# Performance work log

Measured on AMD Instinct MI355X. Metric: run time of the kernel, lower is better.

The kernel has to match this reference:

```python
import math
import jax, jax.numpy as jnp
import numpy as np

# ---- constants (module-level in the original source) ----
_CMAG_A = 0.75
_CMAG_B = 120.0
_CMAG_K = 17.3
_DEG2RAD = math.pi / 180.0
AMP = 100.0
_SPREAD = math.sqrt(AMP / 675.0)
VIEW_ANGLE = 90.0
MAP_SIZE = 256
SOFT_MATCH_SIGMA = 1.5
RENDER_CHUNK = 50
N_SHANK = 10            # N_CONTACTPOINTS_SHANK -> 10^3 = 1000 contacts
SPACING = 0.4           # SPACING_ALONG_XY (mm)


def setup_inputs() -> dict:
    key = jax.random.key(0)
    ks = jax.random.split(key, 12)
    B, V, N = 8, 10000, N_SHANK ** 3
    # bounded params: alpha, beta, offset, shank_length
    alpha = jax.random.uniform(ks[0], (B,), minval=-60.0, maxval=60.0)
    beta = jax.random.uniform(ks[1], (B,), minval=0.0, maxval=90.0)
    offset = jax.random.uniform(ks[2], (B,), minval=0.0, maxval=3.0)
    shank = jax.random.uniform(ks[3], (B,), minval=8.0, maxval=12.0)
    params = jnp.stack([alpha, beta, offset, shank], axis=-1).astype(jnp.float32)
    electrode_logits = jax.random.normal(ks[4], (B, N), dtype=jnp.float32)
    start_loc = jnp.array([30.0, -40.0, 10.0], dtype=jnp.float32)
    # V1 voxel positions clustered around the insertion start point
    v1_pos = start_loc + jax.random.uniform(ks[5], (V, 3), minval=-25.0, maxval=25.0)
    pol = jax.random.uniform(ks[6], (V,), minval=0.0, maxval=360.0)
    ecc = jax.random.uniform(ks[7], (V,), minval=0.2, maxval=12.0)
    sig = jax.random.uniform(ks[8], (V,), minval=0.5, maxval=3.0)
    v1_prf = jnp.stack([pol, ecc, sig], axis=-1).astype(jnp.float32)
    surf_dist_lut = jax.random.uniform(ks[9], (37, 26), minval=10.0, maxval=20.0)
    alpha_grid = jnp.linspace(-90.0, 90.0, 37, dtype=jnp.float32)
    beta_grid = jnp.linspace(-15.0, 110.0, 26, dtype=jnp.float32)
    # contact grid template [n^3, 3] = (x, y, z_frac)
    yv = jnp.arange(N_SHANK, dtype=jnp.float32) * SPACING
    xv = jnp.arange(N_SHANK, dtype=jnp.float32) * SPACING
    zf = jnp.linspace(0.0, 1.0, N_SHANK, dtype=jnp.float32)
    yy, xx, zz = jnp.meshgrid(yv, xv, zf, indexing='ij')
    grid_template = jnp.stack([xx, yy, zz], axis=-1).reshape(-1, 3)
    return {
        'params': params,
        'electrode_logits': electrode_logits,
        'v1_pos': v1_pos.astype(jnp.float32),
        'v1_prf': v1_prf,
        'start_loc': start_loc,
        'surf_dist_lut': surf_dist_lut.astype(jnp.float32),
        'alpha_grid': alpha_grid,
        'beta_grid': beta_grid,
        'grid_template': grid_template,
    }


def _rotation_matrix(alpha_deg, beta_deg):
    a = alpha_deg * _DEG2RAD
    b = beta_deg * _DEG2RAD
    ca, sa = jnp.cos(a), jnp.sin(a)
    cb, sb = jnp.cos(b), jnp.sin(b)
    ones = jnp.ones_like(a)
    zeros = jnp.zeros_like(a)
    Rx = jnp.stack([jnp.stack([ones, zeros, zeros], -1),
                    jnp.stack([zeros, ca, -sa], -1),
                    jnp.stack([zeros, sa, ca], -1)], axis=-2)
    Ry = jnp.stack([jnp.stack([cb, zeros, sb], -1),
                    jnp.stack([zeros, ones, zeros], -1),
                    jnp.stack([-sb, zeros, cb], -1)], axis=-2)
    return Rx @ Ry  # [B,3,3]


def _interp_surface_dist(alpha, beta, lut, a_grid, b_grid):
    # bilinear grid_sample with align_corners=True + border padding == clamped
    # pixel-space bilinear interpolation
    na, nb = lut.shape
    a_norm = 2.0 * (alpha - a_grid[0]) / (a_grid[-1] - a_grid[0] + 1e-08) - 1.0
    b_norm = 2.0 * (beta - b_grid[0]) / (b_grid[-1] - b_grid[0] + 1e-08) - 1.0
    ai = jnp.clip((a_norm + 1.0) * 0.5 * (na - 1), 0.0, na - 1.0)
    bi = jnp.clip((b_norm + 1.0) * 0.5 * (nb - 1), 0.0, nb - 1.0)
    a0 = jnp.clip(jnp.floor(ai), 0, na - 1).astype(jnp.int32)
    b0 = jnp.clip(jnp.floor(bi), 0, nb - 1).astype(jnp.int32)
    a1 = jnp.minimum(a0 + 1, na - 1)
    b1 = jnp.minimum(b0 + 1, nb - 1)
    fa = ai - a0.astype(ai.dtype)
    fb = bi - b0.astype(bi.dtype)
    v00 = lut[a0, b0]; v01 = lut[a0, b1]; v10 = lut[a1, b0]; v11 = lut[a1, b1]
    out = (v00 * (1 - fa) * (1 - fb) + v01 * (1 - fa) * fb
           + v10 * fa * (1 - fb) + v11 * fa * fb)
    return jnp.maximum(out, 1.0)


def _forward(params, electrode_logits, v1_pos, v1_prf, start_loc,
             surf_dist_lut, alpha_grid, beta_grid, grid_template):
    B = params.shape[0]
    N = grid_template.shape[0]
    H = W = MAP_SIZE
    alpha, beta, offset, shank = (params[:, 0], params[:, 1], params[:, 2], params[:, 3])
    elec_prob = jax.nn.sigmoid(electrode_logits)

    # ---- positioned contact grid [B,N,3] ----
    xy = jnp.broadcast_to(grid_template[None, :, :2], (B, N, 2))
    z = grid_template[None, :, 2:3] * shank[:, None, None]
    grid = jnp.concatenate([xy, z], axis=-1)
    grid = grid - grid.mean(axis=1, keepdims=True)
    R = _rotation_matrix(alpha, beta)
    rotated = jnp.einsum('bnc,bdc->bnd', grid, R)   # grid @ R^T
    ref = jnp.array([0.0, 0.0, -1.0], dtype=params.dtype)
    direction = jnp.einsum('bij,j->bi', R, ref)
    direction = direction / jnp.linalg.norm(direction, axis=-1, keepdims=True)
    surf_dist = _interp_surface_dist(alpha, beta, surf_dist_lut, alpha_grid, beta_grid)
    penetration = surf_dist - shank / 2.0 - offset
    grid_center = start_loc[None, :] + direction * penetration[:, None]
    contact_pos = rotated + grid_center[:, None, :]

    # ---- soft PRF lookup via gaussian kernel matching (avoid [B,N,V,3] diff) ----
    p2 = jnp.sum(contact_pos ** 2, axis=-1)          # [B,N]
    v2 = jnp.sum(v1_pos ** 2, axis=-1)               # [V]
    cross = jnp.einsum('bnc,vc->bnv', contact_pos, v1_pos)
    d2 = jnp.maximum(p2[:, :, None] + v2[None, None, :] - 2.0 * cross, 0.0)
    weights = jnp.exp(-d2 / (2.0 * SOFT_MATCH_SIGMA ** 2))   # [B,N,V]
    wsum = weights.sum(axis=-1)
    validity = jnp.minimum(wsum, 1.0)
    weights_norm = weights / (wsum[:, :, None] + 1e-08)
    prf = jnp.einsum('bnv,vp->bnp', weights_norm, v1_prf)    # [B,N,3]

    # ---- chunked gaussian splatting -> [B,1,H,W] ----
    angle_rad = prf[:, :, 0] * _DEG2RAD
    ecc = prf[:, :, 1]
    m = _CMAG_K * (1.0 / (ecc + _CMAG_A) - 1.0 / (ecc + _CMAG_B))
    m_inv = 1.0 / (jnp.abs(m) + 1e-08)
    phos_sigma = _SPREAD * m_inv / 2.0
    scaled_ecc = H / VIEW_ANGLE
    cx = ecc * jnp.cos(angle_rad) * scaled_ecc + H / 2.0
    cy = ecc * jnp.sin(angle_rad) * scaled_ecc + W / 2.0
    phos_size = jnp.maximum(phos_sigma * scaled_ecc, 1.0)
    w = elec_prob * validity

    gy, gx = jnp.meshgrid(jnp.arange(H, dtype=params.dtype),
                          jnp.arange(W, dtype=params.dtype), indexing='ij')
    n_chunks = N // RENDER_CHUNK
    def to_chunks(t):  # [B,N] -> [n_chunks,B,chunk]
        return t.reshape(B, n_chunks, RENDER_CHUNK).transpose(1, 0, 2)
    scan_in = (to_chunks(cx), to_chunks(cy), to_chunks(phos_size), to_chunks(w))

    def body(acc, ch):
        cx_, cy_, s_, w_ = ch  # [B,chunk]
        g = jnp.exp(-((gx[None, None] - cx_[:, :, None, None]) ** 2
                      + (gy[None, None] - cy_[:, :, None, None]) ** 2)
                    / (s_[:, :, None, None] ** 2 + 1e-08))
        return acc + jnp.einsum('bchw,bc->bhw', g, w_), None

    phos_map, _ = jax.lax.scan(body, jnp.zeros((B, H, W), dtype=params.dtype), scan_in)
    phos_map = jnp.rot90(phos_map, k=1, axes=(-2, -1))
    max_val = phos_map.reshape(B, -1).max(axis=1)[:, None, None]
    phos_map = phos_map / (max_val + 1e-08)
    return phos_map[:, None, :, :]


def reference(params, electrode_logits, v1_pos, v1_prf, start_loc,
              surf_dist_lut, alpha_grid, beta_grid, grid_template):
    return _forward(params, electrode_logits, v1_pos, v1_prf, start_loc,
                    surf_dist_lut, alpha_grid, beta_grid, grid_template)
```

## Files before the change

### kernel.cpp

```cpp
#include <hip/hip_runtime.h>
#include <math.h>

#define WS_MAP    0
#define WS_CNT    524416
#define WS_EPOS   524736
#define WS_CPOS   557504
#define WS_CPRF   885184
#define WS_PART   1049024
#define WS_MAX    1704384

#define NB 8
#define NN 1000
#define NV 10000
#define NSEG 40
#define NSEG2 20
#define SEGCAP 256
#define NEB 1024

__global__ __launch_bounds__(256) void k_cull(const float* __restrict__ params,
                                              const float* __restrict__ start_loc,
                                              const float* __restrict__ lut,
                                              const float* __restrict__ agrid,
                                              const float* __restrict__ bgrid,
                                              const float* __restrict__ v1_pos,
                                              const float* __restrict__ v1_prf,
                                              const float* __restrict__ tmpl,
                                              float* __restrict__ ws) {
    __shared__ float sst[NB*16];
    __shared__ int   lcnt[NB];
    int g = blockIdx.x, t = threadIdx.x;
    int v = g*256 + t;
    float4* mp = (float4*)(ws + WS_MAP);
    #pragma unroll
    for (int k = 0; k < 13; ++k) {
        int idx = k*10240 + v;
        if (idx < 131072) mp[idx] = make_float4(0.f,0.f,0.f,0.f);
    }
    if (g == 0 && t < NB) ws[WS_MAX + t] = 0.f;
    if (t < NB) lcnt[t] = 0;
    if (t < NB) {
        int b = t;
        float alpha = params[b*4+0], beta = params[b*4+1];
        float off   = params[b*4+2], shank = params[b*4+3];
        const float D2R = 0.017453292519943295f;
        float a = alpha*D2R, bb = beta*D2R;
        float ca = cosf(a), sa = sinf(a), cb = cosf(bb), sb = sinf(bb);
        float r00=cb,     r01=0.f, r02=sb;
        float r10=sa*sb,  r11=ca,  r12=-sa*cb;
        float r20=-ca*sb, r21=sa,  r22=ca*cb;
        float dx=-r02, dy=-r12, dz=-r22;
        float inv = rsqrtf(dx*dx+dy*dy+dz*dz);
        dx*=inv; dy*=inv; dz*=inv;
        float ag0=agrid[0], agN=agrid[36], bg0=bgrid[0], bgN=bgrid[25];
        float an = 2.f*(alpha-ag0)/(agN-ag0+1e-8f) - 1.f;
        float bn = 2.f*(beta -bg0)/(bgN-bg0+1e-8f) - 1.f;
        float ai = fminf(fmaxf((an+1.f)*0.5f*36.f, 0.f), 36.f);
        float bi = fminf(fmaxf((bn+1.f)*0.5f*25.f, 0.f), 25.f);
        int a0 = (int)floorf(ai); a0 = a0<0?0:(a0>36?36:a0);
        int b0 = (int)floorf(bi); b0 = b0<0?0:(b0>25?25:b0);
        int a1 = a0+1>36?36:a0+1;
        int b1 = b0+1>25?25:b0+1;
        float fa = ai - (float)a0, fb = bi - (float)b0;
        float v00=lut[a0*26+b0], v01=lut[a0*26+b1], v10=lut[a1*26+b0], v11=lut[a1*26+b1];
        float sd = v00*(1.f-fa)*(1.f-fb) + v01*(1.f-fa)*fb + v10*fa*(1.f-fb) + v11*fa*fb;
        sd = fmaxf(sd, 1.f);
        float pen = sd - shank*0.5f - off;
        float hs = shank*0.5f;
        sst[b*16+0]=r00; sst[b*16+1]=r01; sst[b*16+2]=r02;
        sst[b*16+3]=r10; sst[b*16+4]=r11; sst[b*16+5]=r12;
        sst[b*16+6]=r20; sst[b*16+7]=r21; sst[b*16+8]=r22;
        sst[b*16+9]  = start_loc[0] + dx*pen;
        sst[b*16+10] = start_loc[1] + dy*pen;
        sst[b*16+11] = start_loc[2] + dz*pen;
        sst[b*16+12] = shank;
        sst[b*16+13] = fabsf(r00)*1.8f + fabsf(r01)*1.8f + fabsf(r02)*hs;
        sst[b*16+14] = fabsf(r10)*1.8f + fabsf(r11)*1.8f + fabsf(r12)*hs;
        sst[b*16+15] = fabsf(r20)*1.8f + fabsf(r21)*1.8f + fabsf(r22)*hs;
    }
    __syncthreads();
    const float C = -0.32059889797532524f;
    if (v < 8192) {
        float4* ep = (float4*)(ws + WS_EPOS);
        if (v < NB*NN) {
            int b = v/1000, n = v - b*1000;
            const float* st = sst + b*16;
            float gx = tmpl[n*3]-1.8f, gy = tmpl[n*3+1]-1.8f;
            float gz = (tmpl[n*3+2]-0.5f)*st[12];
            float px = st[0]*gx + st[1]*gy + st[2]*gz + st[9];
            float py = st[3]*gx + st[4]*gy + st[5]*gz + st[10];
            float pz = st[6]*gx + st[7]*gy + st[8]*gz + st[11];
            ep[v] = make_float4(px, py, pz, C*(px*px+py*py+pz*pz));
        } else {
            ep[v] = make_float4(0.f, 0.f, 0.f, -1e30f);
        }
    }
    bool valid = v < NV;
    float x=0.f, y=0.f, z=0.f, pol=0.f, ecc=0.f;
    if (valid) {
        x = v1_pos[v*3]; y = v1_pos[v*3+1]; z = v1_pos[v*3+2];
        pol = v1_prf[v*3]; ecc = v1_prf[v*3+1];
    }
    float4 payload = make_float4(-2.f*C*x, -2.f*C*y, -2.f*C*z, C*(x*x+y*y+z*z));
    int lane = t & 63;
    float4* cpos = (float4*)(ws + WS_CPOS);
    float2* cprf = (float2*)(ws + WS_CPRF);
    #pragma unroll
    for (int b = 0; b < NB; ++b) {
        const float* st = sst + b*16;
        float dxc = fmaxf(fabsf(x - st[9])  - st[13], 0.f);
        float dyc = fmaxf(fabsf(y - st[10]) - st[14], 0.f);
        float dzc = fmaxf(fabsf(z - st[11]) - st[15], 0.f);
        bool pred = valid && (dxc*dxc + dyc*dyc + dzc*dzc <= 90.f);
        unsigned long long m = __ballot(pred);
        int base = 0;
        if (lane == 0) base = atomicAdd(&lcnt[b], (int)__popcll(m));
        base = __shfl(base, 0, 64);
        if (pred) {
            int my = base + (int)__popcll(m & ((1ull << lane) - 1ull));
            int slot = b*10240 + g*SEGCAP + my;
            cpos[slot] = payload;
            cprf[slot] = make_float2(pol, ecc);
        }
    }
    __syncthreads();
    if (t < NB) ((int*)(ws + WS_CNT))[g*NB + t] = lcnt[t];
}

__global__ __launch_bounds__(256) void k_match(float* __restrict__ ws) {
    __shared__ float4 sq[2*SEGCAP];
    __shared__ float2 spe[2*SEGCAP];
    int g = blockIdx.x, t = threadIdx.x;
    int b = g / 40, r = g - b*40, qp = r >> 1, eg = r & 1;
    int q0 = qp*2, q1 = qp*2 + 1;
    const int* cnt = (const int*)(ws + WS_CNT);
    int c0 = cnt[q0*NB + b], c1 = cnt[q1*NB + b];
    const float4* cpos = (const float4*)(ws + WS_CPOS);
    const float2* cprf = (const float2*)(ws + WS_CPRF);
    if (t < c0) {
        sq[t]  = cpos[b*10240 + q0*SEGCAP + t];
        spe[t] = cprf[b*10240 + q0*SEGCAP + t];
    }
    if (t < c1) {
        sq[c0 + t]  = cpos[b*10240 + q1*SEGCAP + t];
        spe[c0 + t] = cprf[b*10240 + q1*SEGCAP + t];
    }
    __syncthreads();
    int cq = c0 + c1;
    const float4* ep = (const float4*)(ws + WS_EPOS);
    int n0 = eg*512 + t, n1 = n0 + 256;
    float4 P0 = (n0 < NN) ? ep[b*NN + n0] : make_float4(0.f,0.f,0.f,-1e30f);
    float4 P1 = (n1 < NN) ? ep[b*NN + n1] : make_float4(0.f,0.f,0.f,-1e30f);
    float sw0=0.f,sp0=0.f,se0=0.f, sw1=0.f,sp1=0.f,se1=0.f;
    #pragma unroll 2
    for (int i = 0; i < cq; ++i) {
        float4 qq = sq[i];
        float2 pe = spe[i];
        float a0 = fmaf(qq.x, P0.x, fmaf(qq.y, P0.y, fmaf(qq.z, P0.z, P0.w + qq.w)));
        float w0 = __builtin_amdgcn_exp2f(a0);
        sw0 += w0; sp0 = fmaf(w0, pe.x, sp0); se0 = fmaf(w0, pe.y, se0);
        float a1 = fmaf(qq.x, P1.x, fmaf(qq.y, P1.y, fmaf(qq.z, P1.z, P1.w + qq.w)));
        float w1 = __builtin_amdgcn_exp2f(a1);
        sw1 += w1; sp1 = fmaf(w1, pe.x, sp1); se1 = fmaf(w1, pe.y, se1);
    }
    float4* part = (float4*)(ws + WS_PART);
    int baseq = (b*NSEG2 + qp)*NEB;
    part[baseq + n0] = make_float4(sw0, sp0, se0, 0.f);
    part[baseq + n1] = make_float4(sw1, sp1, se1, 0.f);
}

__global__ __launch_bounds__(256) void k_prender(const float* __restrict__ logits,
                                                 float* __restrict__ ws) {
    __shared__ float4 red[4][64];
    __shared__ float4 par[64];
    __shared__ float  mred[4];
    int g = blockIdx.x, t = threadIdx.x, lane = t & 63, w = t >> 6;
    int b = g >> 4, E0 = (g & 15) * 64;
    const float4* part = (const float4*)(ws + WS_PART);
    int el = E0 + lane;
    float sw = 0.f, sp = 0.f, se = 0.f;
    #pragma unroll
    for (int i = 0; i < 5; ++i) {
        float4 p = part[(b*NSEG2 + (w + i*4))*NEB + el];
        sw += p.x; sp += p.y; se += p.z;
    }
    red[w][lane] = make_float4(sw, sp, se, 0.f);
    __syncthreads();
    if (w == 0) {
        float4 a = red[0][lane], b4 = red[1][lane], c4 = red[2][lane], d4 = red[3][lane];
        sw = (a.x+b4.x) + (c4.x+d4.x);
        sp = (a.y+b4.y) + (c4.y+d4.y);
        se = (a.z+b4.z) + (c4.z+d4.z);
        float denom = sw + 1e-8f;
        float pol = sp/denom, eccv = se/denom;
        float validity = fminf(sw, 1.f);
        int n = E0 + lane;
        float lg = (n < NN) ? logits[b*NN + n] : 0.f;
        float prob = 1.f/(1.f + __expf(-lg));
        float wgt = (n < NN) ? prob * validity : 0.f;
        float ang = pol * 0.017453292519943295f;
        float m1 = 17.3f*(1.f/(eccv+0.75f) - 1.f/(eccv+120.f));
        float minv = 1.f/(fabsf(m1)+1e-8f);
        float sig  = 0.3849001794597506f * minv * 0.5f;
        const float scl = 256.f/90.f;
        float s = fmaxf(sig*scl, 1.f);
        float invden = 1.f/(s*s + 1e-8f);
        par[lane] = make_float4(eccv*__cosf(ang)*scl + 128.f,
                                eccv*__sinf(ang)*scl + 128.f, invden, wgt);
    }
    __syncthreads();
    int ix = lane & 7, iy = lane >> 3;
    float mx = 0.f;
    for (int k = 0; k < 16; ++k) {
        int el2 = k*4 + w;
        float4 P = par[el2];
        if (P.w <= 0.f) continue;
        int fx = (int)floorf(P.x), fy = (int)floorf(P.y);
        int X = fx - 3 + ix, Y = fy - 3 + iy;
        if (X >= 0 && X < 256 && Y >= 0 && Y < 256) {
            float dx = (float)X - P.x, dy = (float)Y - P.y;
            float d2 = dx*dx + dy*dy;
            if (d2 <= 12.25f) {
                float val = P.w * __expf(-d2 * P.z);
                float old = atomicAdd(ws + WS_MAP + b*65536 + Y*256 + X, val);
                mx = fmaxf(mx, old + val);
            }
        }
    }
    #pragma unroll
    for (int s2 = 32; s2 >= 1; s2 >>= 1) mx = fmaxf(mx, __shfl_xor(mx, s2, 64));
    if (lane == 0) mred[w] = mx;
    __syncthreads();
    if (t == 0) {
        mx = fmaxf(fmaxf(mred[0], mred[1]), fmaxf(mred[2], mred[3]));
        atomicMax((unsigned int*)(ws + WS_MAX + b), __float_as_uint(mx));
    }
}

__global__ __launch_bounds__(256) void k_final(const float* __restrict__ ws,
                                               float* __restrict__ out) {
    __shared__ float tile[32][33];
    int g  = blockIdx.x;
    int b  = g >> 6;
    int t6 = g & 63;
    int r0 = (t6 >> 3) * 32;
    int c0 = (t6 & 7) * 32;
    int ic0 = 224 - r0;
    int j  = threadIdx.x & 31;
    int i0 = threadIdx.x >> 5;
    const float* m = ws + WS_MAP + b*65536;
    #pragma unroll
    for (int p = 0; p < 4; ++p) {
        int i = i0 + p*8;
        tile[i][j] = m[(c0+i)*256 + ic0 + j];
    }
    __syncthreads();
    float inv = 1.f/(ws[WS_MAX + b] + 1e-8f);
    #pragma unroll
    for (int p = 0; p < 4; ++p) {
        int k = i0 + p*8;
        out[b*65536 + (r0+k)*256 + c0 + j] = tile[j][31-k] * inv;
    }
}

extern "C" void kernel_launch(void* const* d_in, const int* in_sizes, int n_in,
                              void* d_out, int out_size, void* d_ws, size_t ws_size,
                              hipStream_t stream) {
    const float* params    = (const float*)d_in[0];
    const float* logits    = (const float*)d_in[1];
    const float* v1_pos    = (const float*)d_in[2];
    const float* v1_prf    = (const float*)d_in[3];
    const float* start_loc = (const float*)d_in[4];
    const float* lut       = (const float*)d_in[5];
    const float* agrid     = (const float*)d_in[6];
    const float* bgrid     = (const float*)d_in[7];
    const float* tmpl      = (const float*)d_in[8];
    float* ws  = (float*)d_ws;
    float* out = (float*)d_out;

    k_cull   <<<40,  256, 0, stream>>>(params, start_loc, lut, agrid, bgrid,
                                       v1_pos, v1_prf, tmpl, ws);
    k_match  <<<320, 256, 0, stream>>>(ws);
    k_prender<<<128, 256, 0, stream>>>(logits, ws);
    k_final  <<<512, 256, 0, stream>>>(ws, out);
}
```

Measured before the change: 101.8 us.

## Fuse pipeline into one cooperative kernel with tile-local shared-memory splatting

Merges the four kernels (cull, match, prender, final) into a single cooperative launch of 320 blocks, with grid.sync between stages. The render stage now splats each block's 32x64 output tile into shared memory, using a per-tile culled element list, rather than doing global atomics into a zeroed map. This removes the full-map zeroing and the separate rotate/normalise pass. It aims to cut launch overhead and global atomic and memory traffic, at the cost of grid-wide barriers and fewer active blocks in the later stages.

```diff
diff --git a/kernel.cpp b/kernel.cpp
--- a/kernel.cpp
+++ b/kernel.cpp
@@ -1,13 +1,8 @@
 #include <hip/hip_runtime.h>
+#include <hip/hip_cooperative_groups.h>
 #include <math.h>
 
-#define WS_MAP    0
-#define WS_CNT    524416
-#define WS_EPOS   524736
-#define WS_CPOS   557504
-#define WS_CPRF   885184
-#define WS_PART   1049024
-#define WS_MAX    1704384
+namespace cg = cooperative_groups;
 
 #define NB 8
 #define NN 1000
@@ -17,248 +12,274 @@
 #define SEGCAP 256
 #define NEB 1024
 
-__global__ __launch_bounds__(256) void k_cull(const float* __restrict__ params,
-                                              const float* __restrict__ start_loc,
-                                              const float* __restrict__ lut,
-                                              const float* __restrict__ agrid,
-                                              const float* __restrict__ bgrid,
-                                              const float* __restrict__ v1_pos,
-                                              const float* __restrict__ v1_prf,
-                                              const float* __restrict__ tmpl,
-                                              float* __restrict__ ws) {
-    __shared__ float sst[NB*16];
-    __shared__ int   lcnt[NB];
-    int g = blockIdx.x, t = threadIdx.x;
-    int v = g*256 + t;
-    float4* mp = (float4*)(ws + WS_MAP);
-    #pragma unroll
-    for (int k = 0; k < 13; ++k) {
-        int idx = k*10240 + v;
-        if (idx < 131072) mp[idx] = make_float4(0.f,0.f,0.f,0.f);
-    }
-    if (g == 0 && t < NB) ws[WS_MAX + t] = 0.f;
-    if (t < NB) lcnt[t] = 0;
-    if (t < NB) {
-        int b = t;
-        float alpha = params[b*4+0], beta = params[b*4+1];
-        float off   = params[b*4+2], shank = params[b*4+3];
-        const float D2R = 0.017453292519943295f;
-        float a = alpha*D2R, bb = beta*D2R;
-        float ca = cosf(a), sa = sinf(a), cb = cosf(bb), sb = sinf(bb);
-        float r00=cb,     r01=0.f, r02=sb;
-        float r10=sa*sb,  r11=ca,  r12=-sa*cb;
-        float r20=-ca*sb, r21=sa,  r22=ca*cb;
-        float dx=-r02, dy=-r12, dz=-r22;
-        float inv = rsqrtf(dx*dx+dy*dy+dz*dz);
-        dx*=inv; dy*=inv; dz*=inv;
-        float ag0=agrid[0], agN=agrid[36], bg0=bgrid[0], bgN=bgrid[25];
-        float an = 2.f*(alpha-ag0)/(agN-ag0+1e-8f) - 1.f;
-        float bn = 2.f*(beta -bg0)/(bgN-bg0+1e-8f) - 1.f;
-        float ai = fminf(fmaxf((an+1.f)*0.5f*36.f, 0.f), 36.f);
-        float bi = fminf(fmaxf((bn+1.f)*0.5f*25.f, 0.f), 25.f);
-        int a0 = (int)floorf(ai); a0 = a0<0?0:(a0>36?36:a0);
-        int b0 = (int)floorf(bi); b0 = b0<0?0:(b0>25?25:b0);
-        int a1 = a0+1>36?36:a0+1;
-        int b1 = b0+1>25?25:b0+1;
-        float fa = ai - (float)a0, fb = bi - (float)b0;
-        float v00=lut[a0*26+b0], v01=lut[a0*26+b1], v10=lut[a1*26+b0], v11=lut[a1*26+b1];
-        float sd = v00*(1.f-fa)*(1.f-fb) + v01*(1.f-fa)*fb + v10*fa*(1.f-fb) + v11*fa*fb;
-        sd = fmaxf(sd, 1.f);
-        float pen = sd - shank*0.5f - off;
-        float hs = shank*0.5f;
-        sst[b*16+0]=r00; sst[b*16+1]=r01; sst[b*16+2]=r02;
-        sst[b*16+3]=r10; sst[b*16+4]=r11; sst[b*16+5]=r12;
-        sst[b*16+6]=r20; sst[b*16+7]=r21; sst[b*16+8]=r22;
-        sst[b*16+9]  = start_loc[0] + dx*pen;
-        sst[b*16+10] = start_loc[1] + dy*pen;
-        sst[b*16+11] = start_loc[2] + dz*pen;
-        sst[b*16+12] = shank;
-        sst[b*16+13] = fabsf(r00)*1.8f + fabsf(r01)*1.8f + fabsf(r02)*hs;
-        sst[b*16+14] = fabsf(r10)*1.8f + fabsf(r11)*1.8f + fabsf(r12)*hs;
-        sst[b*16+15] = fabsf(r20)*1.8f + fabsf(r21)*1.8f + fabsf(r22)*hs;
-    }
-    __syncthreads();
-    const float C = -0.32059889797532524f;
-    if (v < 8192) {
-        float4* ep = (float4*)(ws + WS_EPOS);
-        if (v < NB*NN) {
-            int b = v/1000, n = v - b*1000;
+#define WS_CNT  0
+#define WS_EPOS 512
+#define WS_CPOS 33280
+#define WS_CPRF 360960
+#define WS_PART 524800
+#define WS_PAR  1180160
+#define WS_MAX  1212928
+
+__global__ __launch_bounds__(256, 2) void k_fused(
+    const float* __restrict__ params,
+    const float* __restrict__ logits,
+    const float* __restrict__ v1_pos,
+    const float* __restrict__ v1_prf,
+    const float* __restrict__ start_loc,
+    const float* __restrict__ lut,
+    const float* __restrict__ agrid,
+    const float* __restrict__ bgrid,
+    const float* __restrict__ tmpl,
+    float* __restrict__ ws,
+    float* __restrict__ out)
+{
+    cg::grid_group grid = cg::this_grid();
+    __shared__ __align__(16) unsigned char smem[12544];
+    const int g = blockIdx.x, t = threadIdx.x;
+    const int lane = t & 63, w = t >> 6;
+
+    if (g < NSEG) {
+        float* sst = (float*)smem;
+        int*   lcnt = (int*)(smem + 512);
+        if (t < NB) lcnt[t] = 0;
+        if (t < NB) {
+            int b = t;
+            float alpha = params[b*4+0], beta = params[b*4+1];
+            float off   = params[b*4+2], shank = params[b*4+3];
+            const float D2R = 0.017453292519943295f;
+            float a = alpha*D2R, bb = beta*D2R;
+            float ca = cosf(a), sa = sinf(a), cb = cosf(bb), sb = sinf(bb);
+            float r00=cb,     r01=0.f, r02=sb;
+            float r10=sa*sb,  r11=ca,  r12=-sa*cb;
+            float r20=-ca*sb, r21=sa,  r22=ca*cb;
+            float dx=-r02, dy=-r12, dz=-r22;
+            float inv = rsqrtf(dx*dx+dy*dy+dz*dz);
+            dx*=inv; dy*=inv; dz*=inv;
+            float ag0=agrid[0], agN=agrid[36], bg0=bgrid[0], bgN=bgrid[25];
+            float an = 2.f*(alpha-ag0)/(agN-ag0+1e-8f) - 1.f;
+            float bn = 2.f*(beta -bg0)/(bgN-bg0+1e-8f) - 1.f;
+            float ai = fminf(fmaxf((an+1.f)*0.5f*36.f, 0.f), 36.f);
+            float bi = fminf(fmaxf((bn+1.f)*0.5f*25.f, 0.f), 25.f);
+            int a0 = (int)floorf(ai); a0 = a0<0?0:(a0>36?36:a0);
+            int b0 = (int)floorf(bi); b0 = b0<0?0:(b0>25?25:b0);
+            int a1 = a0+1>36?36:a0+1;
+            int b1 = b0+1>25?25:b0+1;
+            float fa = ai - (float)a0, fb = bi - (float)b0;
+            float v00=lut[a0*26+b0], v01=lut[a0*26+b1], v10=lut[a1*26+b0], v11=lut[a1*26+b1];
+            float sd = v00*(1.f-fa)*(1.f-fb) + v01*(1.f-fa)*fb + v10*fa*(1.f-fb) + v11*fa*fb;
+            sd = fmaxf(sd, 1.f);
+            float pen = sd - shank*0.5f - off;
+            float hs = shank*0.5f;
+            sst[b*16+0]=r00; sst[b*16+1]=r01; sst[b*16+2]=r02;
+            sst[b*16+3]=r10; sst[b*16+4]=r11; sst[b*16+5]=r12;
+            sst[b*16+6]=r20; sst[b*16+7]=r21; sst[b*16+8]=r22;
+            sst[b*16+9]  = start_loc[0] + dx*pen;
+            sst[b*16+10] = start_loc[1] + dy*pen;
+            sst[b*16+11] = start_loc[2] + dz*pen;
+            sst[b*16+12] = shank;
+            sst[b*16+13] = fabsf(r00)*1.8f + fabsf(r01)*1.8f + fabsf(r02)*hs;
+            sst[b*16+14] = fabsf(r10)*1.8f + fabsf(r11)*1.8f + fabsf(r12)*hs;
+            sst[b*16+15] = fabsf(r20)*1.8f + fabsf(r21)*1.8f + fabsf(r22)*hs;
+        }
+        __syncthreads();
+        const float C = -0.32059889797532524f;
+        int v = g*256 + t;
+        if (v < 8192) {
+            float4* ep = (float4*)(ws + WS_EPOS);
+            if (v < NB*NN) {
+                int b = v/1000, n = v - b*1000;
+                const float* st = sst + b*16;
+                float gx = tmpl[n*3]-1.8f, gy = tmpl[n*3+1]-1.8f;
+                float gz = (tmpl[n*3+2]-0.5f)*st[12];
+                float px = st[0]*gx + st[1]*gy + st[2]*gz + st[9];
+                float py = st[3]*gx + st[4]*gy + st[5]*gz + st[10];
+                float pz = st[6]*gx + st[7]*gy + st[8]*gz + st[11];
+                ep[v] = make_float4(px, py, pz, C*(px*px+py*py+pz*pz));
+            } else {
+                ep[v] = make_float4(0.f, 0.f, 0.f, -1e30f);
+            }
+        }
+        bool valid = v < NV;
+        float x=0.f, y=0.f, z=0.f, pol=0.f, ecc=0.f;
+        if (valid) {
+            x = v1_pos[v*3]; y = v1_pos[v*3+1]; z = v1_pos[v*3+2];
+            pol = v1_prf[v*3]; ecc = v1_prf[v*3+1];
+        }
+        float4 payload = make_float4(-2.f*C*x, -2.f*C*y, -2.f*C*z, C*(x*x+y*y+z*z));
+        float4* cpos = (float4*)(ws + WS_CPOS);
+        float2* cprf = (float2*)(ws + WS_CPRF);
+        #pragma unroll
+        for (int b = 0; b < NB; ++b) {
             const float* st = sst + b*16;
-            float gx = tmpl[n*3]-1.8f, gy = tmpl[n*3+1]-1.8f;
-            float gz = (tmpl[n*3+2]-0.5f)*st[12];
-            float px = st[0]*gx + st[1]*gy + st[2]*gz + st[9];
-            float py = st[3]*gx + st[4]*gy + st[5]*gz + st[10];
-            float pz = st[6]*gx + st[7]*gy + st[8]*gz + st[11];
-            ep[v] = make_float4(px, py, pz, C*(px*px+py*py+pz*pz));
-        } else {
-            ep[v] = make_float4(0.f, 0.f, 0.f, -1e30f);
-        }
-    }
-    bool valid = v < NV;
-    float x=0.f, y=0.f, z=0.f, pol=0.f, ecc=0.f;
-    if (valid) {
-        x = v1_pos[v*3]; y = v1_pos[v*3+1]; z = v1_pos[v*3+2];
-        pol = v1_prf[v*3]; ecc = v1_prf[v*3+1];
-    }
-    float4 payload = make_float4(-2.f*C*x, -2.f*C*y, -2.f*C*z, C*(x*x+y*y+z*z));
-    int lane = t & 63;
-    float4* cpos = (float4*)(ws + WS_CPOS);
-    float2* cprf = (float2*)(ws + WS_CPRF);
-    #pragma unroll
-    for (int b = 0; b < NB; ++b) {
-        const float* st = sst + b*16;
-        float dxc = fmaxf(fabsf(x - st[9])  - st[13], 0.f);
-        float dyc = fmaxf(fabsf(y - st[10]) - st[14], 0.f);
-        float dzc = fmaxf(fabsf(z - st[11]) - st[15], 0.f);
-        bool pred = valid && (dxc*dxc + dyc*dyc + dzc*dzc <= 90.f);
-        unsigned long long m = __ballot(pred);
-        int base = 0;
-        if (lane == 0) base = atomicAdd(&lcnt[b], (int)__popcll(m));
-        base = __shfl(base, 0, 64);
-        if (pred) {
-            int my = base + (int)__popcll(m & ((1ull << lane) - 1ull));
-            int slot = b*10240 + g*SEGCAP + my;
-            cpos[slot] = payload;
-            cprf[slot] = make_float2(pol, ecc);
-        }
-    }
-    __syncthreads();
-    if (t < NB) ((int*)(ws + WS_CNT))[g*NB + t] = lcnt[t];
-}
-
-__global__ __launch_bounds__(256) void k_match(float* __restrict__ ws) {
-    __shared__ float4 sq[2*SEGCAP];
-    __shared__ float2 spe[2*SEGCAP];
-    int g = blockIdx.x, t = threadIdx.x;
-    int b = g / 40, r = g - b*40, qp = r >> 1, eg = r & 1;
-    int q0 = qp*2, q1 = qp*2 + 1;
-    const int* cnt = (const int*)(ws + WS_CNT);
-    int c0 = cnt[q0*NB + b], c1 = cnt[q1*NB + b];
-    const float4* cpos = (const float4*)(ws + WS_CPOS);
-    const float2* cprf = (const float2*)(ws + WS_CPRF);
-    if (t < c0) {
-        sq[t]  = cpos[b*10240 + q0*SEGCAP + t];
-        spe[t] = cprf[b*10240 + q0*SEGCAP + t];
-    }
-    if (t < c1) {
-        sq[c0 + t]  = cpos[b*10240 + q1*SEGCAP + t];
-        spe[c0 + t] = cprf[b*10240 + q1*SEGCAP + t];
-    }
-    __syncthreads();
-    int cq = c0 + c1;
-    const float4* ep = (const float4*)(ws + WS_EPOS);
-    int n0 = eg*512 + t, n1 = n0 + 256;
-    float4 P0 = (n0 < NN) ? ep[b*NN + n0] : make_float4(0.f,0.f,0.f,-1e30f);
-    float4 P1 = (n1 < NN) ? ep[b*NN + n1] : make_float4(0.f,0.f,0.f,-1e30f);
-    float sw0=0.f,sp0=0.f,se0=0.f, sw1=0.f,sp1=0.f,se1=0.f;
-    #pragma unroll 2
-    for (int i = 0; i < cq; ++i) {
-        float4 qq = sq[i];
-        float2 pe = spe[i];
-        float a0 = fmaf(qq.x, P0.x, fmaf(qq.y, P0.y, fmaf(qq.z, P0.z, P0.w + qq.w)));
-        float w0 = __builtin_amdgcn_exp2f(a0);
-        sw0 += w0; sp0 = fmaf(w0, pe.x, sp0); se0 = fmaf(w0, pe.y, se0);
-        float a1 = fmaf(qq.x, P1.x, fmaf(qq.y, P1.y, fmaf(qq.z, P1.z, P1.w + qq.w)));
-        float w1 = __builtin_amdgcn_exp2f(a1);
-        sw1 += w1; sp1 = fmaf(w1, pe.x, sp1); se1 = fmaf(w1, pe.y, se1);
-    }
-    float4* part = (float4*)(ws + WS_PART);
-    int baseq = (b*NSEG2 + qp)*NEB;
-    part[baseq + n0] = make_float4(sw0, sp0, se0, 0.f);
-    part[baseq + n1] = make_float4(sw1, sp1, se1, 0.f);
-}
-
-__global__ __launch_bounds__(256) void k_prender(const float* __restrict__ logits,
-                                                 float* __restrict__ ws) {
-    __shared__ float4 red[4][64];
-    __shared__ float4 par[64];
-    __shared__ float  mred[4];
-    int g = blockIdx.x, t = threadIdx.x, lane = t & 63, w = t >> 6;
-    int b = g >> 4, E0 = (g & 15) * 64;
-    const float4* part = (const float4*)(ws + WS_PART);
-    int el = E0 + lane;
-    float sw = 0.f, sp = 0.f, se = 0.f;
-    #pragma unroll
-    for (int i = 0; i < 5; ++i) {
-        float4 p = part[(b*NSEG2 + (w + i*4))*NEB + el];
-        sw += p.x; sp += p.y; se += p.z;
-    }
-    red[w][lane] = make_float4(sw, sp, se, 0.f);
-    __syncthreads();
-    if (w == 0) {
-        float4 a = red[0][lane], b4 = red[1][lane], c4 = red[2][lane], d4 = red[3][lane];
-        sw = (a.x+b4.x) + (c4.x+d4.x);
-        sp = (a.y+b4.y) + (c4.y+d4.y);
-        se = (a.z+b4.z) + (c4.z+d4.z);
-        float denom = sw + 1e-8f;
-        float pol = sp/denom, eccv = se/denom;
-        float validity = fminf(sw, 1.f);
-        int n = E0 + lane;
-        float lg = (n < NN) ? logits[b*NN + n] : 0.f;
-        float prob = 1.f/(1.f + __expf(-lg));
-        float wgt = (n < NN) ? prob * validity : 0.f;
-        float ang = pol * 0.017453292519943295f;
-        float m1 = 17.3f*(1.f/(eccv+0.75f) - 1.f/(eccv+120.f));
-        float minv = 1.f/(fabsf(m1)+1e-8f);
-        float sig  = 0.3849001794597506f * minv * 0.5f;
-        const float scl = 256.f/90.f;
-        float s = fmaxf(sig*scl, 1.f);
-        float invden = 1.f/(s*s + 1e-8f);
-        par[lane] = make_float4(eccv*__cosf(ang)*scl + 128.f,
-                                eccv*__sinf(ang)*scl + 128.f, invden, wgt);
-    }
-    __syncthreads();
-    int ix = lane & 7, iy = lane >> 3;
-    float mx = 0.f;
-    for (int k = 0; k < 16; ++k) {
-        int el2 = k*4 + w;
-        float4 P = par[el2];
-        if (P.w <= 0.f) continue;
-        int fx = (int)floorf(P.x), fy = (int)floorf(P.y);
-        int X = fx - 3 + ix, Y = fy - 3 + iy;
-        if (X >= 0 && X < 256 && Y >= 0 && Y < 256) {
-            float dx = (float)X - P.x, dy = (float)Y - P.y;
-            float d2 = dx*dx + dy*dy;
-            if (d2 <= 12.25f) {
-                float val = P.w * __expf(-d2 * P.z);
-                float old = atomicAdd(ws + WS_MAP + b*65536 + Y*256 + X, val);
-                mx = fmaxf(mx, old + val);
+            float dxc = fmaxf(fabsf(x - st[9])  - st[13], 0.f);
+            float dyc = fmaxf(fabsf(y - st[10]) - st[14], 0.f);
+            float dzc = fmaxf(fabsf(z - st[11]) - st[15], 0.f);
+            bool pred = valid && (dxc*dxc + dyc*dyc + dzc*dzc <= 90.f);
+            unsigned long long m = __ballot(pred);
+            int base = 0;
+            if (lane == 0) base = atomicAdd(&lcnt[b], (int)__popcll(m));
+            base = __shfl(base, 0, 64);
+            if (pred) {
+                int my = base + (int)__popcll(m & ((1ull << lane) - 1ull));
+                int slot = b*10240 + g*SEGCAP + my;
+                cpos[slot] = payload;
+                cprf[slot] = make_float2(pol, ecc);
             }
         }
-    }
-    #pragma unroll
-    for (int s2 = 32; s2 >= 1; s2 >>= 1) mx = fmaxf(mx, __shfl_xor(mx, s2, 64));
-    if (lane == 0) mred[w] = mx;
-    __syncthreads();
-    if (t == 0) {
-        mx = fmaxf(fmaxf(mred[0], mred[1]), fmaxf(mred[2], mred[3]));
-        atomicMax((unsigned int*)(ws + WS_MAX + b), __float_as_uint(mx));
-    }
-}
-
-__global__ __launch_bounds__(256) void k_final(const float* __restrict__ ws,
-                                               float* __restrict__ out) {
-    __shared__ float tile[32][33];
-    int g  = blockIdx.x;
-    int b  = g >> 6;
-    int t6 = g & 63;
-    int r0 = (t6 >> 3) * 32;
-    int c0 = (t6 & 7) * 32;
-    int ic0 = 224 - r0;
-    int j  = threadIdx.x & 31;
-    int i0 = threadIdx.x >> 5;
-    const float* m = ws + WS_MAP + b*65536;
-    #pragma unroll
-    for (int p = 0; p < 4; ++p) {
-        int i = i0 + p*8;
-        tile[i][j] = m[(c0+i)*256 + ic0 + j];
-    }
-    __syncthreads();
-    float inv = 1.f/(ws[WS_MAX + b] + 1e-8f);
-    #pragma unroll
-    for (int p = 0; p < 4; ++p) {
-        int k = i0 + p*8;
-        out[b*65536 + (r0+k)*256 + c0 + j] = tile[j][31-k] * inv;
+        __syncthreads();
+        if (t < NB) ((int*)(ws + WS_CNT))[g*NB + t] = lcnt[t];
+    } else if (g == NSEG) {
+        if (t < NB) ws[WS_MAX + t] = 0.f;
+    }
+
+    grid.sync();
+    {
+        float4* sq  = (float4*)smem;
+        float2* spe = (float2*)(smem + 8192);
+        int b = g / 40, r = g - b*40, qp = r >> 1, eg = r & 1;
+        int q0 = qp*2, q1 = q0 + 1;
+        const int* cnt = (const int*)(ws + WS_CNT);
+        int c0 = cnt[q0*NB + b], c1 = cnt[q1*NB + b];
+        const float4* cpos = (const float4*)(ws + WS_CPOS);
+        const float2* cprf = (const float2*)(ws + WS_CPRF);
+        if (t < c0) {
+            sq[t]  = cpos[b*10240 + q0*SEGCAP + t];
+            spe[t] = cprf[b*10240 + q0*SEGCAP + t];
+        }
+        if (t < c1) {
+            sq[c0 + t]  = cpos[b*10240 + q1*SEGCAP + t];
+            spe[c0 + t] = cprf[b*10240 + q1*SEGCAP + t];
+        }
+        __syncthreads();
+        int cq = c0 + c1;
+        const float4* ep = (const float4*)(ws + WS_EPOS);
+        int n0 = eg*512 + t, n1 = n0 + 256;
+        float4 P0 = (n0 < NN) ? ep[b*NN + n0] : make_float4(0.f,0.f,0.f,-1e30f);
+        float4 P1 = (n1 < NN) ? ep[b*NN + n1] : make_float4(0.f,0.f,0.f,-1e30f);
+        float sw0=0.f,sp0=0.f,se0=0.f, sw1=0.f,sp1=0.f,se1=0.f;
+        #pragma unroll 2
+        for (int i = 0; i < cq; ++i) {
+            float4 qq = sq[i];
+            float2 pe = spe[i];
+            float a0 = fmaf(qq.x, P0.x, fmaf(qq.y, P0.y, fmaf(qq.z, P0.z, P0.w + qq.w)));
+            float w0 = __builtin_amdgcn_exp2f(a0);
+            sw0 += w0; sp0 = fmaf(w0, pe.x, sp0); se0 = fmaf(w0, pe.y, se0);
+            float a1 = fmaf(qq.x, P1.x, fmaf(qq.y, P1.y, fmaf(qq.z, P1.z, P1.w + qq.w)));
+            float w1 = __builtin_amdgcn_exp2f(a1);
+            sw1 += w1; sp1 = fmaf(w1, pe.x, sp1); se1 = fmaf(w1, pe.y, se1);
+        }
+        float4* part = (float4*)(ws + WS_PART);
+        int baseq = (b*NSEG2 + qp)*NEB;
+        part[baseq + n0] = make_float4(sw0, sp0, se0, 0.f);
+        part[baseq + n1] = make_float4(sw1, sp1, se1, 0.f);
+    }
+
+    grid.sync();
+    if (g < 128) {
+        float4* red = (float4*)smem;
+        int b = g >> 4, E0 = (g & 15) * 64;
+        const float4* part = (const float4*)(ws + WS_PART);
+        int el = E0 + lane;
+        float sw = 0.f, sp = 0.f, se = 0.f;
+        #pragma unroll
+        for (int i = 0; i < 5; ++i) {
+            float4 p = part[(b*NSEG2 + (w + i*4))*NEB + el];
+            sw += p.x; sp += p.y; se += p.z;
+        }
+        red[w*64 + lane] = make_float4(sw, sp, se, 0.f);
+        __syncthreads();
+        if (w == 0) {
+            float4 a = red[lane], b4 = red[64+lane], c4 = red[128+lane], d4 = red[192+lane];
+            sw = (a.x+b4.x) + (c4.x+d4.x);
+            sp = (a.y+b4.y) + (c4.y+d4.y);
+            se = (a.z+b4.z) + (c4.z+d4.z);
+            float denom = sw + 1e-8f;
+            float pol = sp/denom, eccv = se/denom;
+            float validity = fminf(sw, 1.f);
+            int n = E0 + lane;
+            float lg = (n < NN) ? logits[b*NN + n] : 0.f;
+            float prob = 1.f/(1.f + __expf(-lg));
+            float wgt = (n < NN) ? prob * validity : 0.f;
+            float ang = pol * 0.017453292519943295f;
+            float m1 = 17.3f*(1.f/(eccv+0.75f) - 1.f/(eccv+120.f));
+            float minv = 1.f/(fabsf(m1)+1e-8f);
+            float sig  = 0.3849001794597506f * minv * 0.5f;
+            const float scl = 256.f/90.f;
+            float s = fmaxf(sig*scl, 1.f);
+            float invden = 1.f/(s*s + 1e-8f);
+            ((float4*)(ws + WS_PAR))[b*NEB + E0 + lane] =
+                make_float4(eccv*__cosf(ang)*scl + 128.f,
+                            eccv*__sinf(ang)*scl + 128.f, invden, wgt);
+        }
+    }
+
+    grid.sync();
+    float* tile = (float*)smem;
+    unsigned short* elist = (unsigned short*)(smem + 8320);
+    int*   ecnt = (int*)(smem + 8320 + 2048);
+    float* mred = (float*)(smem + 8320 + 2048 + 16);
+    const int bR = g >> 5, tt = g & 31;
+    const int y0 = (tt & 3) * 64, x0 = (tt >> 2) * 32;
+    if (g < 256) {
+        for (int i = t; i < 32*65; i += 256) tile[i] = 0.f;
+        if (t == 0) *ecnt = 0;
+        __syncthreads();
+        const float4* par = (const float4*)(ws + WS_PAR) + bR*NEB;
+        #pragma unroll
+        for (int rd = 0; rd < 4; ++rd) {
+            int e = rd*256 + t;
+            float4 P = par[e];
+            bool hit = P.w > 0.f;
+            if (hit) {
+                float fx = floorf(P.x), fy = floorf(P.y);
+                hit = (fx >= (float)(x0-4)) && (fx <= (float)(x0+34))
+                   && (fy >= (float)(y0-4)) && (fy <= (float)(y0+66));
+            }
+            unsigned long long m = __ballot(hit);
+            int base = 0;
+            if (lane == 0) base = atomicAdd(ecnt, (int)__popcll(m));
+            base = __shfl(base, 0, 64);
+            if (hit) elist[base + (int)__popcll(m & ((1ull << lane) - 1ull))] = (unsigned short)e;
+        }
+        __syncthreads();
+        int n = *ecnt;
+        int ix = lane & 7, iy = lane >> 3;
+        for (int i = w; i < n; i += 4) {
+            float4 P = par[elist[i]];
+            int fx = (int)floorf(P.x), fy = (int)floorf(P.y);
+            int X = fx - 3 + ix, Y = fy - 3 + iy;
+            int xl = X - x0, yl = Y - y0;
+            if (xl >= 0 && xl < 32 && yl >= 0 && yl < 64) {
+                float dx = (float)X - P.x, dy = (float)Y - P.y;
+                float d2 = dx*dx + dy*dy;
+                if (d2 <= 12.25f) {
+                    atomicAdd(&tile[xl*65 + yl], P.w * __expf(-d2 * P.z));
+                }
+            }
+        }
+        __syncthreads();
+        float mx = 0.f;
+        for (int i = t; i < 32*65; i += 256) mx = fmaxf(mx, tile[i]);
+        #pragma unroll
+        for (int s2 = 32; s2 >= 1; s2 >>= 1) mx = fmaxf(mx, __shfl_xor(mx, s2, 64));
+        if (lane == 0) mred[w] = mx;
+        __syncthreads();
+        if (t == 0) {
+            mx = fmaxf(fmaxf(mred[0], mred[1]), fmaxf(mred[2], mred[3]));
+            atomicMax((unsigned int*)(ws + WS_MAX + bR), __float_as_uint(mx));
+        }
+    }
+
+    grid.sync();
+    if (g < 256) {
+        float inv = 1.f / (ws[WS_MAX + bR] + 1e-8f);
+        int rx = t >> 3, sg = (t & 7) * 8;
+        const float* tp = tile + rx*65 + sg;
+        float* op = out + bR*65536 + (255 - (x0 + rx))*256 + y0 + sg;
+        float4 o0 = make_float4(tp[0]*inv, tp[1]*inv, tp[2]*inv, tp[3]*inv);
+        float4 o1 = make_float4(tp[4]*inv, tp[5]*inv, tp[6]*inv, tp[7]*inv);
+        ((float4*)op)[0] = o0;
+        ((float4*)op)[1] = o1;
     }
 }
 
@@ -277,9 +298,11 @@
     float* ws  = (float*)d_ws;
     float* out = (float*)d_out;
 
-    k_cull   <<<40,  256, 0, stream>>>(params, start_loc, lut, agrid, bgrid,
-                                       v1_pos, v1_prf, tmpl, ws);
-    k_match  <<<320, 256, 0, stream>>>(ws);
-    k_prender<<<128, 256, 0, stream>>>(logits, ws);
-    k_final  <<<512, 256, 0, stream>>>(ws, out);
+    void* kargs[] = {
+        (void*)&params, (void*)&logits, (void*)&v1_pos, (void*)&v1_prf,
+        (void*)&start_loc, (void*)&lut, (void*)&agrid, (void*)&bgrid,
+        (void*)&tmpl, (void*)&ws, (void*)&out
+    };
+    hipLaunchCooperativeKernel((const void*)k_fused, dim3(320), dim3(256),
+                               kargs, 0, stream);
 }
```

After: 302.0 us. +196.7%, slower.
